# Optimization experiments

Hardware: AMD Instinct MI355X
Metric: run time of the kernel (lower is better)

The kernel has to match this reference:

```python
import jax, jax.numpy as jnp
import numpy as np

R = 4        # downsample / window size
HEADS = 8
TOPK = 4


def _dwconv3x3(x_nchw, w, b):
    # depthwise 3x3, padding 1. w: [C,1,3,3]
    C = x_nchw.shape[1]
    y = jax.lax.conv_general_dilated(
        x_nchw, w, window_strides=(1, 1), padding=((1, 1), (1, 1)),
        dimension_numbers=('NCHW', 'OIHW', 'NCHW'), feature_group_count=C)
    return y + b[None, :, None, None]


def setup_inputs() -> dict:
    key = jax.random.key(0)
    ks = jax.random.split(key, 8)
    B, H, W, C = 8, 64, 64, 384
    s = 0.02
    return {
        'x': jax.random.normal(ks[0], (B, H, W, C), jnp.float32),
        'qkv_w': jax.random.normal(ks[1], (3 * C, C), jnp.float32) * s,
        'dwx_w': jax.random.normal(ks[2], (C, 1, 3, 3), jnp.float32) * s,
        'dwx_b': jax.random.normal(ks[3], (C,), jnp.float32) * s,
        'dw_w': jax.random.normal(ks[4], (C, 1, 3, 3), jnp.float32) * s,
        'dw_b': jax.random.normal(ks[5], (C,), jnp.float32) * s,
        'pw_w': jax.random.normal(ks[6], (C, C), jnp.float32) * s,
        'pw_b': jax.random.normal(ks[7], (C,), jnp.float32) * s,
    }


def reference(x, qkv_w, dwx_w, dwx_b, dw_w, dw_b, pw_w, pw_b):
    B, H, W, C = x.shape
    h, r, topk = HEADS, R, TOPK
    d = C // h
    scale = d ** -0.5
    Hc, Wc = H // r, W // r
    Nc = Hc * Wc

    y = x

    # ---- coarse stream: avg-pool downsample then dense attention ----
    xc = x.reshape(B, Hc, r, Wc, r, C).mean(axis=(2, 4))       # [B,Hc,Wc,C]
    xc = xc.reshape(B, Nc, C)
    qkv = (xc @ qkv_w.T).reshape(B, Nc, 3, h, d).transpose(2, 0, 3, 1, 4)
    q, k, v = qkv[0], qkv[1], qkv[2]                           # [B,h,Nc,d]
    attn = jnp.einsum('bhqd,bhkd->bhqk', q, k) * scale         # [B,h,Nc,Nc]
    _, indices = jax.lax.top_k(attn, topk)                     # [B,h,Nc,topk]
    attn = jax.nn.softmax(attn, axis=-1)
    xo = jnp.einsum('bhqk,bhkd->bhqd', attn, v)                # [B,h,Nc,d]
    xo = xo.transpose(0, 2, 1, 3).reshape(B, Hc, Wc, C)

    # ---- full-res stream: windowed sparse attention driven by topk indices ----
    yf = y.reshape(B, H * W, C)
    QKV = (yf @ qkv_w.T).reshape(B, H * W, 3, h, d).transpose(2, 0, 3, 1, 4)
    Q, K, V = QKV[0], QKV[1], QKV[2]                           # [B,h,H*W,d]

    def to_windows(t):
        # [B,h,H*W,d] -> [B,h,nWin,r*r,d], window order matches coarse (h w) flatten
        t = t.reshape(B, h, Hc, r, Wc, r, d).transpose(0, 1, 2, 4, 3, 5, 6)
        return t.reshape(B, h, Nc, r * r, d)

    Qw, Kw, Vw = to_windows(Q), to_windows(K), to_windows(V)

    idx = indices[:, :, :, :, None, None]                      # [B,h,Nc,topk,1,1]
    Kg = jnp.take_along_axis(Kw[:, :, None], idx, axis=3)      # [B,h,Nc,topk,r*r,d]
    Vg = jnp.take_along_axis(Vw[:, :, None], idx, axis=3)
    Kg = Kg.reshape(B, h, Nc, topk * r * r, d)
    Vg = Vg.reshape(B, h, Nc, topk * r * r, d)

    a2 = jnp.einsum('bhnqd,bhnkd->bhnqk', Qw, Kg) * scale
    a2 = jax.nn.softmax(a2, axis=-1)
    yo = jnp.einsum('bhnqk,bhnkd->bhnqd', a2, Vg)              # [B,h,Nc,r*r,d]
    yo = yo.reshape(B, h, Hc, Wc, r, r, d).transpose(0, 2, 4, 3, 5, 1, 6)
    yo = yo.reshape(B, H, W, C)                                # NHWC

    # ---- coarse branch: nearest upsample + depthwise conv ----
    xn = xo.transpose(0, 3, 1, 2)                              # [B,C,Hc,Wc]
    xn = jnp.repeat(jnp.repeat(xn, r, axis=2), r, axis=3)      # [B,C,H,W]
    xn = _dwconv3x3(xn, dwx_w, dwx_b)
    xn = xn.transpose(0, 2, 3, 1)                              # NHWC

    # ---- fuse, depthwise + pointwise conv ----
    z = 0.5 * xn + 0.5 * yo
    z = z.transpose(0, 3, 1, 2)                                # NCHW
    z = _dwconv3x3(z, dw_w, dw_b)
    z = jnp.einsum('bchw,oc->bohw', z, pw_w) + pw_b[None, :, None, None]
    return z.transpose(0, 2, 3, 1)                             # NHWC
```

## Files before the change

### kernel.cpp

```cpp
#include <hip/hip_runtime.h>
#include <hip/hip_bf16.h>


#define Bq 8
#define Hh 8
#define Dd 48
#define Cc 384
#define NC 256
#define MFINE 32768
#define KDIM 384
#define SCALE 0.14433756729740643f

typedef __attribute__((ext_vector_type(8))) short short8;
typedef __attribute__((ext_vector_type(4))) short short4v;
typedef __attribute__((ext_vector_type(4))) float floatx4;

#define QKVW_PLANE 12582912

#define WS_XBF   88342528
#define WS_XC     9437184
#define WS_WQKV 113508352
#define WS_WDWX 114393088
#define WS_BDWX 114400000
#define WS_WDW  114400768
#define WS_BDW  114407680
#define WS_WPW  114408448
#define WS_BPW  114703360

__global__ __launch_bounds__(256) void k_detect(const ushort* x, int* flag) {
    __shared__ int cnt;
    if (threadIdx.x == 0) cnt = 0;
    __syncthreads();
    int c = 0;
    for (int i = threadIdx.x; i < 8192; i += 256) {
        int e = (x[i] >> 7) & 0xFF;
        if (e >= 0xC1) c++;
    }
    atomicAdd(&cnt, c);
    __syncthreads();
    if (threadIdx.x == 0) *flag = (cnt > 16) ? 1 : 0;
}

__device__ __forceinline__ void cvt_seg(const void* src, __hip_bfloat16* dst, int blk, int n4, int fl) {
    int i = blk * 256 + threadIdx.x;
    if (i >= n4) return;
    if (fl) {
        floatx4 v = ((const floatx4*)src)[i];
        short4v o;
        for (int t = 0; t < 4; t++) {
            __hip_bfloat16 hb = __float2bfloat16(v[t]);
            o[t] = *(short*)&hb;
        }
        ((short4v*)dst)[i] = o;
    } else {
        ((short4v*)dst)[i] = ((const short4v*)src)[i];
    }
}

__global__ __launch_bounds__(256) void k_cvt_pool(
        const void* sx, const void* s1, const void* s2, const void* s3,
        const void* s4, const void* s5, const void* s6, const void* s7,
        char* ws, const int* flag) {
    int blk = blockIdx.x;
    int fl = *flag;
    if (blk < 12288) { cvt_seg(sx, (__hip_bfloat16*)(ws + WS_XBF),  blk,          3145728, fl); return; }
    if (blk < 12720) { cvt_seg(s1, (__hip_bfloat16*)(ws + WS_WQKV), blk - 12288,  110592, fl); return; }
    if (blk < 12724) { cvt_seg(s2, (__hip_bfloat16*)(ws + WS_WDWX), blk - 12720,  864,    fl); return; }
    if (blk < 12725) { cvt_seg(s3, (__hip_bfloat16*)(ws + WS_BDWX), blk - 12724,  96,     fl); return; }
    if (blk < 12729) { cvt_seg(s4, (__hip_bfloat16*)(ws + WS_WDW),  blk - 12725,  864,    fl); return; }
    if (blk < 12730) { cvt_seg(s5, (__hip_bfloat16*)(ws + WS_BDW),  blk - 12729,  96,     fl); return; }
    if (blk < 12874) { cvt_seg(s6, (__hip_bfloat16*)(ws + WS_WPW),  blk - 12730,  36864,  fl); return; }
    if (blk < 12875) { cvt_seg(s7, (__hip_bfloat16*)(ws + WS_BPW),  blk - 12874,  96,     fl); return; }
    int pb = blk - 12875;
    if (threadIdx.x >= 192) return;
    int b = pb >> 8, n = pb & 255;
    int yc = n >> 4, xcc = n & 15;
    int c0 = threadIdx.x * 2;
    size_t pixbase = (((size_t)(b * 64 + yc * 4)) * 64 + xcc * 4) * Cc + c0;
    float s0 = 0.f, s1v = 0.f;
    if (fl) {
        const float* xf = (const float*)sx;
        for (int i = 0; i < 4; i++)
            for (int j = 0; j < 4; j++) {
                float2 u = *(const float2*)(xf + pixbase + ((size_t)i * 64 + j) * Cc);
                s0 += u.x; s1v += u.y;
            }
    } else {
        const ushort* xb = (const ushort*)sx;
        for (int i = 0; i < 4; i++)
            for (int j = 0; j < 4; j++) {
                uint u = *(const uint*)(xb + pixbase + ((size_t)i * 64 + j) * Cc);
                s0 += __uint_as_float(u << 16);
                s1v += __uint_as_float(u & 0xFFFF0000u);
            }
    }
    __hip_bfloat16 h0 = __float2bfloat16(s0 * 0.0625f), h1 = __float2bfloat16(s1v * 0.0625f);
    uint uo = (uint)*(ushort*)&h0 | ((uint)*(ushort*)&h1 << 16);
    *(uint*)((ushort*)(ws + WS_XC) + (size_t)pb * Cc + c0) = uo;
}

__device__ __forceinline__ void gload_lds16(const ushort* g, short* l) {
    __builtin_amdgcn_global_load_lds(
        (const __attribute__((address_space(1))) unsigned int*)(g),
        (__attribute__((address_space(3))) unsigned int*)(l), 16, 0, 0);
}

__device__ __forceinline__ void gemm128_dbuf(const ushort* A, const ushort* B,
                                             int tile_m, int tile_n,
                                             short* As, short* Bs, floatx4 (&acc)[4][4]) {
    int lane = threadIdx.x & 63, wave = threadIdx.x >> 6;
    int m_off = (wave >> 1) * 64, n_off = (wave & 1) * 64;
    int row16 = lane & 15, quad = lane >> 4;
    int srow = lane >> 3;
    int scol = (((lane & 7) ^ srow) * 8);
    for (int i = 0; i < 4; i++)
        for (int j = 0; j < 4; j++)
            acc[i][j] = (floatx4){0.f, 0.f, 0.f, 0.f};
    int rsw = (row16 & 7) * 8;
#define STG(buf, k0)                                                                          \
    for (int g = wave; g < 16; g += 4) {                                                      \
        gload_lds16(A + (size_t)(tile_m + g * 8 + srow) * KDIM + (k0) + scol, As + (buf) * 8192 + g * 512); \
        gload_lds16(B + (size_t)(tile_n + g * 8 + srow) * KDIM + (k0) + scol, Bs + (buf) * 8192 + g * 512); \
    }
    STG(0, 0)
    int cur = 0;
    for (int k0 = 0; k0 < KDIM; k0 += 64) {
        if (k0 + 64 < KDIM) {
            STG(cur ^ 1, k0 + 64)
            asm volatile("s_waitcnt vmcnt(8)" ::: "memory");
        } else {
            asm volatile("s_waitcnt vmcnt(0)" ::: "memory");
        }
        __builtin_amdgcn_s_barrier();
        __builtin_amdgcn_sched_barrier(0);
        const short* Ab = As + cur * 8192;
        const short* Bb = Bs + cur * 8192;
        for (int h = 0; h < 2; h++) {
            short8 af[4], bf[4];
            for (int mt = 0; mt < 4; mt++)
                af[mt] = *(const short8*)(Ab + (m_off + mt * 16 + row16) * 64 + (((h * 4 + quad) * 8) ^ rsw));
            for (int nt = 0; nt < 4; nt++)
                bf[nt] = *(const short8*)(Bb + (n_off + nt * 16 + row16) * 64 + (((h * 4 + quad) * 8) ^ rsw));
            for (int mt = 0; mt < 4; mt++)
                for (int nt = 0; nt < 4; nt++)
                    acc[mt][nt] = __builtin_amdgcn_mfma_f32_16x16x32_bf16(af[mt], bf[nt], acc[mt][nt], 0, 0, 0);
        }
        __builtin_amdgcn_sched_barrier(0);
        __builtin_amdgcn_s_barrier();
        cur ^= 1;
    }
#undef STG
}

__device__ __forceinline__ void gemm128_sb(const ushort* A, const ushort* B,
                                           int tile_m, int tile_n,
                                           short* As, short* Bs, floatx4 (&acc)[4][4]) {
    int lane = threadIdx.x & 63, wave = threadIdx.x >> 6;
    int m_off = (wave >> 1) * 64, n_off = (wave & 1) * 64;
    int row16 = lane & 15, quad = lane >> 4;
    int srow = lane >> 3;
    int scol = (((lane & 7) ^ srow) * 8);
    for (int i = 0; i < 4; i++)
        for (int j = 0; j < 4; j++)
            acc[i][j] = (floatx4){0.f, 0.f, 0.f, 0.f};
    int rsw = (row16 & 7) * 8;
    for (int k0 = 0; k0 < KDIM; k0 += 64) {
        for (int g = wave; g < 16; g += 4) {
            gload_lds16(A + (size_t)(tile_m + g * 8 + srow) * KDIM + k0 + scol, As + g * 512);
            gload_lds16(B + (size_t)(tile_n + g * 8 + srow) * KDIM + k0 + scol, Bs + g * 512);
        }
        __syncthreads();
        for (int h = 0; h < 2; h++) {
            short8 af[4], bf[4];
            for (int mt = 0; mt < 4; mt++)
                af[mt] = *(const short8*)(As + (m_off + mt * 16 + row16) * 64 + (((h * 4 + quad) * 8) ^ rsw));
            for (int nt = 0; nt < 4; nt++)
                bf[nt] = *(const short8*)(Bs + (n_off + nt * 16 + row16) * 64 + (((h * 4 + quad) * 8) ^ rsw));
            for (int mt = 0; mt < 4; mt++)
                for (int nt = 0; nt < 4; nt++)
                    acc[mt][nt] = __builtin_amdgcn_mfma_f32_16x16x32_bf16(af[mt], bf[nt], acc[mt][nt], 0, 0, 0);
        }
        __syncthreads();
    }
}

__device__ __forceinline__ floatx4 mfma_tile(const ushort* A, const ushort* W,
                                             int tile_m, int tile_n, int lane) {
    int row16 = lane & 15, quad = lane >> 4;
    const ushort* arow = A + (size_t)(tile_m + row16) * KDIM + quad * 8;
    const ushort* brow = W + (size_t)(tile_n + row16) * KDIM + quad * 8;
    floatx4 acc = {0.f, 0.f, 0.f, 0.f};
    for (int kk = 0; kk < KDIM; kk += 32) {
        short8 af = *(const short8*)(arow + kk);
        short8 bf = *(const short8*)(brow + kk);
        acc = __builtin_amdgcn_mfma_f32_16x16x32_bf16(af, bf, acc, 0, 0, 0);
    }
    return acc;
}

__global__ __launch_bounds__(256) void k_gemm_qkv_coarse(const ushort* A, const ushort* W,
                                                         __hip_bfloat16* qh, __hip_bfloat16* ql,
                                                         __hip_bfloat16* kh, __hip_bfloat16* kl,
                                                         __hip_bfloat16* vt) {
    int lane = threadIdx.x & 63, wave = threadIdx.x >> 6;
    int tile_m = blockIdx.y * 32 + (wave >> 1) * 16;
    int tile_n = blockIdx.x * 32 + (wave & 1) * 16;
    floatx4 acc = mfma_tile(A, W, tile_m, tile_n, lane);
    int row16 = lane & 15, quad = lane >> 4;
    int n = tile_n + row16;
    int which = n / Cc, hd = n % Cc, head = hd / Dd, dim = hd % Dd;
    for (int rr = 0; rr < 4; rr++) {
        int m = tile_m + quad * 4 + rr;
        int b = m >> 8, nc = m & 255;
        float v = acc[rr];
        __hip_bfloat16 hi = __float2bfloat16(v);
        if (which == 0) {
            size_t p = ((size_t)((b * Hh + head) * NC + nc)) * Dd + dim;
            qh[p] = hi;
            ql[p] = __float2bfloat16(v - __bfloat162float(hi));
        } else if (which == 1) {
            size_t p = ((size_t)((b * Hh + head) * NC + nc)) * Dd + dim;
            kh[p] = hi;
            kl[p] = __float2bfloat16(v - __bfloat162float(hi));
        } else {
            vt[((size_t)((b * Hh + head) * Dd + dim)) * NC + nc] = hi;
        }
    }
}

#define PST 264
__global__ __launch_bounds__(256) void k_coarse_attn(const ushort* qh, const ushort* ql,
                                                     const ushort* kh, const ushort* kl,
                                                     const ushort* vt,
                                                     int* idx_out, __hip_bfloat16* xo) {
    __shared__ __align__(16) short Pl[4][16 * PST];
    int lane = threadIdx.x & 63, wave = threadIdx.x >> 6;
    int bh = blockIdx.x >> 2, qt = blockIdx.x & 3;
    int row16 = lane & 15, quad = lane >> 4;
    int q0 = qt * 64 + wave * 16;
    short8 zf = {0, 0, 0, 0, 0, 0, 0, 0};
    const ushort* qhr = qh + ((size_t)(bh * NC + q0 + row16)) * Dd;
    const ushort* qlr = ql + ((size_t)(bh * NC + q0 + row16)) * Dd;
    short8 aqh0 = *(const short8*)(qhr + quad * 8);
    short8 aqh1 = (quad < 2) ? *(const short8*)(qhr + 32 + quad * 8) : zf;
    short8 aql0 = *(const short8*)(qlr + quad * 8);
    short8 aql1 = (quad < 2) ? *(const short8*)(qlr + 32 + quad * 8) : zf;
    floatx4 s[16];
    for (int nt = 0; nt < 16; nt++) {
        const ushort* khr = kh + ((size_t)(bh * NC + nt * 16 + row16)) * Dd;
        const ushort* klr = kl + ((size_t)(bh * NC + nt * 16 + row16)) * Dd;
        short8 bh0 = *(const short8*)(khr + quad * 8);
        short8 bh1 = (quad < 2) ? *(const short8*)(khr + 32 + quad * 8) : zf;
        short8 bl0 = *(const short8*)(klr + quad * 8);
        short8 bl1 = (quad < 2) ? *(const short8*)(klr + 32 + quad * 8) : zf;
        floatx4 a = {0.f, 0.f, 0.f, 0.f};
        a = __builtin_amdgcn_mfma_f32_16x16x32_bf16(aqh0, bh0, a, 0, 0, 0);
        a = __builtin_amdgcn_mfma_f32_16x16x32_bf16(aqh1, bh1, a, 0, 0, 0);
        a = __builtin_amdgcn_mfma_f32_16x16x32_bf16(aqh0, bl0, a, 0, 0, 0);
        a = __builtin_amdgcn_mfma_f32_16x16x32_bf16(aqh1, bl1, a, 0, 0, 0);
        a = __builtin_amdgcn_mfma_f32_16x16x32_bf16(aql0, bh0, a, 0, 0, 0);
        a = __builtin_amdgcn_mfma_f32_16x16x32_bf16(aql1, bh1, a, 0, 0, 0);
        s[nt] = a;
    }
    for (int rr = 0; rr < 4; rr++) {
        float sv[16];
        for (int nt = 0; nt < 16; nt++) sv[nt] = s[nt][rr] * SCALE;
        int chosen[4] = {-1, -1, -1, -1};
        float rowmax = 0.f;
        for (int it = 0; it < 4; it++) {
            float bv = -3.402823e38f; int bi = 0x7fffffff;
            for (int nt = 0; nt < 16; nt++) {
                int ki = nt * 16 + row16;
                bool skip = (ki == chosen[0]) | (ki == chosen[1]) | (ki == chosen[2]) | (ki == chosen[3]);
                if (!skip && sv[nt] > bv) { bv = sv[nt]; bi = ki; }
            }
            for (int mk = 1; mk < 16; mk <<= 1) {
                float ov = __shfl_xor(bv, mk); int oi = __shfl_xor(bi, mk);
                if (ov > bv || (ov == bv && oi < bi)) { bv = ov; bi = oi; }
            }
            chosen[it] = bi;
            if (it == 0) rowmax = bv;
        }
        if (row16 == 0) {
            int q = q0 + quad * 4 + rr;
            for (int it = 0; it < 4; it++)
                idx_out[((size_t)bh * NC + q) * 4 + it] = chosen[it];
        }
        float ex[16], sum = 0.f;
        for (int nt = 0; nt < 16; nt++) { ex[nt] = __expf(sv[nt] - rowmax); sum += ex[nt]; }
        for (int mk = 1; mk < 16; mk <<= 1) sum += __shfl_xor(sum, mk);
        float inv = 1.f / sum;
        for (int nt = 0; nt < 16; nt++) {
            __hip_bfloat16 hb = __float2bfloat16(ex[nt] * inv);
            Pl[wave][(quad * 4 + rr) * PST + nt * 16 + row16] = *(short*)&hb;
        }
    }
    const ushort* vbase = vt + (size_t)bh * Dd * NC;
    floatx4 o[3];
    for (int i = 0; i < 3; i++) o[i] = (floatx4){0.f, 0.f, 0.f, 0.f};
    for (int k0 = 0; k0 < 256; k0 += 32) {
        short8 pa = *(const short8*)&Pl[wave][row16 * PST + k0 + quad * 8];
        for (int d2 = 0; d2 < 3; d2++) {
            short8 vb = *(const short8*)(vbase + (size_t)(d2 * 16 + row16) * NC + k0 + quad * 8);
            o[d2] = __builtin_amdgcn_mfma_f32_16x16x32_bf16(pa, vb, o[d2], 0, 0, 0);
        }
    }
    int b = bh >> 3, hh = bh & 7;
    for (int rr = 0; rr < 4; rr++) {
        int q = q0 + quad * 4 + rr;
        size_t base = ((size_t)(b * NC + q)) * Cc + hh * Dd;
        for (int d2 = 0; d2 < 3; d2++)
            xo[base + d2 * 16 + row16] = __float2bfloat16(o[d2][rr]);
    }
}

__global__ __launch_bounds__(256) void k_gemm_qkv_fine(const ushort* A, const ushort* W, __hip_bfloat16* qkvw) {
    __shared__ __align__(16) short smem[32768];
    floatx4 acc[4][4];
    int f = blockIdx.x;
    int s = (f & 7) * 288 + (f >> 3);
    int by = s / 9, bx = s - by * 9;
    int tile_m = by * 128, tile_n = bx * 128;
    gemm128_dbuf(A, W, tile_m, tile_n, smem, smem + 16384, acc);
    int lane = threadIdx.x & 63, wave = threadIdx.x >> 6;
    int m_off = (wave >> 1) * 64, n_off = (wave & 1) * 64;
    int row16 = lane & 15, quad = lane >> 4;
    short* epi = smem + wave * 2304;
    int r = lane >> 1, parity = lane & 1;
    for (int half = 0; half < 2; half++) {
        __syncthreads();
        for (int mt2 = 0; mt2 < 2; mt2++) {
            int mt = half * 2 + mt2;
            for (int nt = 0; nt < 4; nt++)
                for (int rr = 0; rr < 4; rr++) {
                    __hip_bfloat16 hb = __float2bfloat16(acc[mt][nt][rr]);
                    epi[(mt2 * 16 + quad * 4 + rr) * 72 + nt * 16 + row16] = *(short*)&hb;
                }
        }
        __syncthreads();
        int m = tile_m + m_off + half * 32 + r;
        int b = m >> 12, pix = m & 4095;
        int y = pix >> 6, x = pix & 63;
        int win = (y >> 2) * 16 + (x >> 2);
        int pos = (y & 3) * 4 + (x & 3);
        size_t mrow = ((size_t)b * Hh * NC * 16 * Dd) + ((size_t)win * 16 + pos) * Dd;
        for (int i = 0; i < 4; i++) {
            int j = parity + 2 * i;
            int n = tile_n + n_off + j * 8;
            int which = n / Cc, hd = n % Cc, head = hd / Dd, dim = hd % Dd;
            short8 val = *(const short8*)(epi + r * 72 + j * 8);
            size_t dst = (size_t)which * QKVW_PLANE + (size_t)head * (NC * 16 * Dd) + mrow + dim;
            *(short8*)((ushort*)qkvw + dst) = val;
        }
    }
}

#define PSTRIDE 80
#define VSTRIDE 72
__global__ __launch_bounds__(256) void k_win_attn(const __hip_bfloat16* qkvw, const int* idx, __hip_bfloat16* yo) {
    __shared__ __align__(16) short Pl[4][16 * PSTRIDE];
    __shared__ __align__(16) short Vt[4][48 * VSTRIDE];
    int lane = threadIdx.x & 63, wave = threadIdx.x >> 6;
    int gw = blockIdx.x * 4 + wave;
    int bh = gw >> 8, n = gw & 255;
    int row16 = lane & 15, quad = lane >> 4;
    const ushort* qb  = (const ushort*)qkvw + (size_t)(bh * NC + n) * 768;
    const ushort* kwb = (const ushort*)qkvw + (size_t)QKVW_PLANE + (size_t)bh * NC * 768;
    const ushort* vwb = (const ushort*)qkvw + 2 * (size_t)QKVW_PLANE + (size_t)bh * NC * 768;
    int sel[4];
    for (int g = 0; g < 4; g++) sel[g] = idx[(size_t)gw * 4 + g];
    const ushort* vrow = vwb + (size_t)sel[quad] * 768 + row16 * 48;
    short8 vv[6];
    for (int i = 0; i < 6; i++) vv[i] = *(const short8*)(vrow + i * 8);
    short8 zf = {0, 0, 0, 0, 0, 0, 0, 0};
    short8 aq0 = *(const short8*)(qb + row16 * 48 + quad * 8);
    short8 aq1 = (quad < 2) ? *(const short8*)(qb + row16 * 48 + 32 + quad * 8) : zf;
    floatx4 s[4];
    for (int nt = 0; nt < 4; nt++) {
        const ushort* kb = kwb + (size_t)sel[nt] * 768 + row16 * 48;
        short8 bk0 = *(const short8*)(kb + quad * 8);
        short8 bk1 = (quad < 2) ? *(const short8*)(kb + 32 + quad * 8) : zf;
        floatx4 a = {0.f, 0.f, 0.f, 0.f};
        a = __builtin_amdgcn_mfma_f32_16x16x32_bf16(aq0, bk0, a, 0, 0, 0);
        a = __builtin_amdgcn_mfma_f32_16x16x32_bf16(aq1, bk1, a, 0, 0, 0);
        s[nt] = a;
    }
    for (int i = 0; i < 6; i++)
        for (int j = 0; j < 8; j++)
            Vt[wave][(i * 8 + j) * VSTRIDE + lane] = vv[i][j];
    for (int rr = 0; rr < 4; rr++) {
        float sv[4];
        float m = -3.402823e38f;
        for (int nt = 0; nt < 4; nt++) { sv[nt] = s[nt][rr] * SCALE; m = fmaxf(m, sv[nt]); }
        for (int msk = 1; msk < 16; msk <<= 1) m = fmaxf(m, __shfl_xor(m, msk));
        float sum = 0.f;
        for (int nt = 0; nt < 4; nt++) { sv[nt] = expf(sv[nt] - m); sum += sv[nt]; }
        for (int msk = 1; msk < 16; msk <<= 1) sum += __shfl_xor(sum, msk);
        float inv = 1.f / sum;
        for (int nt = 0; nt < 4; nt++) {
            __hip_bfloat16 hb = __float2bfloat16(sv[nt] * inv);
            Pl[wave][(quad * 4 + rr) * PSTRIDE + nt * 16 + row16] = *(short*)&hb;
        }
    }
    floatx4 o[3];
    for (int i = 0; i < 3; i++) o[i] = (floatx4){0.f, 0.f, 0.f, 0.f};
    for (int k0 = 0; k0 < 64; k0 += 32) {
        short8 pa = *(const short8*)&Pl[wave][row16 * PSTRIDE + k0 + quad * 8];
        for (int nt2 = 0; nt2 < 3; nt2++) {
            short8 vb = *(const short8*)&Vt[wave][(nt2 * 16 + row16) * VSTRIDE + k0 + quad * 8];
            o[nt2] = __builtin_amdgcn_mfma_f32_16x16x32_bf16(pa, vb, o[nt2], 0, 0, 0);
        }
    }
    int b = bh >> 3, hh = bh & 7;
    int wy = n >> 4, wx = n & 15;
    for (int rr = 0; rr < 4; rr++) {
        int q = quad * 4 + rr;
        int y = wy * 4 + (q >> 2), x = wx * 4 + (q & 3);
        size_t base = (((size_t)(b * 64 + y)) * 64 + x) * Cc + hh * Dd;
        for (int nt2 = 0; nt2 < 3; nt2++)
            yo[base + nt2 * 16 + row16] = __float2bfloat16(o[nt2][rr]);
    }
}

__global__ __launch_bounds__(192) void k_up_mix(const __hip_bfloat16* xo, const __hip_bfloat16* yo,
                                                const __hip_bfloat16* dwx_w, const __hip_bfloat16* dwx_b,
                                                __hip_bfloat16* zpre) {
    int c2 = threadIdx.x, c0 = c2 * 2;
    int blk = blockIdx.x;
    int xc = blk & 7, by = blk >> 3;
    int y = by & 63, b = by >> 6;
    int x0 = xc * 8;
    float w0[9], w1[9];
    for (int k = 0; k < 9; k++) {
        w0[k] = __bfloat162float(dwx_w[c0 * 9 + k]);
        w1[k] = __bfloat162float(dwx_w[(c0 + 1) * 9 + k]);
    }
    float bias0 = __bfloat162float(dwx_b[c0]), bias1 = __bfloat162float(dwx_b[c0 + 1]);
    const __hip_bfloat16* xrow[3];
    for (int di = 0; di < 3; di++) {
        int yy = y + di - 1;
        xrow[di] = (yy >= 0 && yy < 64) ? xo + ((size_t)(b * NC + (yy >> 2) * 16)) * Cc + c0 : nullptr;
    }
    float vL0[3], vL1[3], vM0[3], vM1[3], vR0[3], vR1[3];
    int cm = x0 >> 2;
    for (int di = 0; di < 3; di++) {
        uint um = xrow[di] ? *(const uint*)(xrow[di] + (size_t)cm * Cc) : 0u;
        vM0[di] = __uint_as_float(um << 16); vM1[di] = __uint_as_float(um & 0xFFFF0000u);
        uint ul = (x0 > 0 && xrow[di]) ? *(const uint*)(xrow[di] + (size_t)(cm - 1) * Cc) : 0u;
        vL0[di] = __uint_as_float(ul << 16); vL1[di] = __uint_as_float(ul & 0xFFFF0000u);
        vR0[di] = vM0[di]; vR1[di] = vM1[di];
    }
    size_t obase = (size_t)by * 64 * Cc + c0;
    for (int x = x0; x < x0 + 8; x++) {
        float a0 = bias0, a1 = bias1;
        for (int di = 0; di < 3; di++) {
            a0 += vL0[di] * w0[di * 3] + vM0[di] * w0[di * 3 + 1] + vR0[di] * w0[di * 3 + 2];
            a1 += vL1[di] * w1[di * 3] + vM1[di] * w1[di * 3 + 1] + vR1[di] * w1[di * 3 + 2];
        }
        uint uy = *(const uint*)(yo + obase + (size_t)x * Cc);
        float z0 = 0.5f * a0 + 0.5f * __uint_as_float(uy << 16);
        float z1 = 0.5f * a1 + 0.5f * __uint_as_float(uy & 0xFFFF0000u);
        __hip_bfloat16 h0 = __float2bfloat16(z0), h1 = __float2bfloat16(z1);
        uint uo = (uint)*(ushort*)&h0 | ((uint)*(ushort*)&h1 << 16);
        *(uint*)(zpre + obase + (size_t)x * Cc) = uo;
        for (int di = 0; di < 3; di++) {
            vL0[di] = vM0[di]; vL1[di] = vM1[di];
            vM0[di] = vR0[di]; vM1[di] = vR1[di];
        }
        int nx = x + 2;
        if ((nx & 3) == 0 || nx > 63) {
            int ncol = nx >> 2;
            for (int di = 0; di < 3; di++) {
                uint ur = (nx <= 63 && xrow[di]) ? *(const uint*)(xrow[di] + (size_t)ncol * Cc) : 0u;
                vR0[di] = __uint_as_float(ur << 16); vR1[di] = __uint_as_float(ur & 0xFFFF0000u);
            }
        }
    }
}

__global__ __launch_bounds__(192) void k_dw2(const __hip_bfloat16* zpre, const __hip_bfloat16* dw_w,
                                             const __hip_bfloat16* dw_b, __hip_bfloat16* z) {
    int c2 = threadIdx.x, c0 = c2 * 2;
    int blk = blockIdx.x;
    int xc = blk & 7, by = blk >> 3;
    int y = by & 63, b = by >> 6;
    int x0 = xc * 8;
    float w0[9], w1[9];
    for (int k = 0; k < 9; k++) {
        w0[k] = __bfloat162float(dw_w[c0 * 9 + k]);
        w1[k] = __bfloat162float(dw_w[(c0 + 1) * 9 + k]);
    }
    float bias0 = __bfloat162float(dw_b[c0]), bias1 = __bfloat162float(dw_b[c0 + 1]);
    const __hip_bfloat16* row[3];
    for (int di = 0; di < 3; di++) {
        int yy = y + di - 1;
        row[di] = (yy >= 0 && yy < 64) ? zpre + ((size_t)(b * 64 + yy) * 64) * Cc + c0 : nullptr;
    }
    float pv0[3], pv1[3], cv0[3], cv1[3], f0[3], f1[3];
    for (int di = 0; di < 3; di++) {
        uint up = (x0 > 0 && row[di]) ? *(const uint*)(row[di] + (size_t)(x0 - 1) * Cc) : 0u;
        pv0[di] = __uint_as_float(up << 16); pv1[di] = __uint_as_float(up & 0xFFFF0000u);
        uint uc = row[di] ? *(const uint*)(row[di] + (size_t)x0 * Cc) : 0u;
        cv0[di] = __uint_as_float(uc << 16); cv1[di] = __uint_as_float(uc & 0xFFFF0000u);
        uint uf = row[di] ? *(const uint*)(row[di] + (size_t)(x0 + 1) * Cc) : 0u;
        f0[di] = __uint_as_float(uf << 16); f1[di] = __uint_as_float(uf & 0xFFFF0000u);
    }
    size_t obase = (size_t)by * 64 * Cc + c0;
    for (int x = x0; x < x0 + 8; x++) {
        float nv0[3], nv1[3];
        for (int di = 0; di < 3; di++) { nv0[di] = f0[di]; nv1[di] = f1[di]; }
        int nx = x + 2;
        for (int di = 0; di < 3; di++) {
            uint uf = (nx < 64 && row[di]) ? *(const uint*)(row[di] + (size_t)nx * Cc) : 0u;
            f0[di] = __uint_as_float(uf << 16); f1[di] = __uint_as_float(uf & 0xFFFF0000u);
        }
        float a0 = bias0, a1 = bias1;
        for (int di = 0; di < 3; di++) {
            a0 += pv0[di] * w0[di * 3] + cv0[di] * w0[di * 3 + 1] + nv0[di] * w0[di * 3 + 2];
            a1 += pv1[di] * w1[di * 3] + cv1[di] * w1[di * 3 + 1] + nv1[di] * w1[di * 3 + 2];
        }
        __hip_bfloat16 h0 = __float2bfloat16(a0), h1 = __float2bfloat16(a1);
        uint uo = (uint)*(ushort*)&h0 | ((uint)*(ushort*)&h1 << 16);
        *(uint*)(z + obase + (size_t)x * Cc) = uo;
        for (int di = 0; di < 3; di++) {
            pv0[di] = cv0[di]; pv1[di] = cv1[di];
            cv0[di] = nv0[di]; cv1[di] = nv1[di];
        }
    }
}

__global__ __launch_bounds__(256) void k_gemm_pw(const ushort* Z, const ushort* W, const __hip_bfloat16* bias,
                                                 void* out, const int* flag) {
    __shared__ __align__(16) short smem[16384];
    floatx4 acc[4][4];
    int f = blockIdx.x;
    int s = (f & 7) * 96 + (f >> 3);
    int by = s / 3, bx = s - by * 3;
    int tile_m = by * 128, tile_n = bx * 128;
    gemm128_sb(Z, W, tile_m, tile_n, smem, smem + 8192, acc);
    int lane = threadIdx.x & 63, wave = threadIdx.x >> 6;
    int m_off = (wave >> 1) * 64, n_off = (wave & 1) * 64;
    int row16 = lane & 15, quad = lane >> 4;
    float* epi = (float*)smem + wave * 1216;
    int f32out = *flag;
    int r4 = lane >> 2, c4 = lane & 3;
    for (int mt = 0; mt < 4; mt++) {
        __syncthreads();
        for (int nt = 0; nt < 4; nt++)
            for (int rr = 0; rr < 4; rr++)
                epi[(quad * 4 + rr) * 76 + nt * 16 + row16] = acc[mt][nt][rr];
        __syncthreads();
        int m = tile_m + m_off + mt * 16 + r4;
        for (int i = 0; i < 4; i++) {
            int j = c4 + 4 * i;
            int n0 = tile_n + n_off + j * 4;
            floatx4 v = *(const floatx4*)(epi + r4 * 76 + j * 4);
            short4v bb = *(const short4v*)((const ushort*)bias + n0);
            for (int t = 0; t < 4; t++) {
                short sb = bb[t];
                v[t] += __bfloat162float(*(const __hip_bfloat16*)&sb);
            }
            if (f32out) {
                *(floatx4*)((float*)out + (size_t)m * Cc + n0) = v;
            } else {
                short4v o;
                for (int t = 0; t < 4; t++) { __hip_bfloat16 hb = __float2bfloat16(v[t]); o[t] = *(short*)&hb; }
                *(short4v*)((__hip_bfloat16*)out + (size_t)m * Cc + n0) = o;
            }
        }
    }
}

extern "C" void kernel_launch(void* const* d_in, const int* in_sizes, int n_in,
                              void* d_out, int out_size, void* d_ws, size_t ws_size,
                              hipStream_t stream) {
    char* ws = (char*)d_ws;
    __hip_bfloat16* qhp  = (__hip_bfloat16*)(ws);
    __hip_bfloat16* qlp  = (__hip_bfloat16*)(ws + 1572864);
    __hip_bfloat16* khp  = (__hip_bfloat16*)(ws + 3145728);
    __hip_bfloat16* klp  = (__hip_bfloat16*)(ws + 4718592);
    __hip_bfloat16* vtp  = (__hip_bfloat16*)(ws + 6291456);
    __hip_bfloat16* xc   = (__hip_bfloat16*)(ws + WS_XC);
    int*            idx  = (int*)(ws + 11010048);
    __hip_bfloat16* xo   = (__hip_bfloat16*)(ws + 11272192);
    __hip_bfloat16* qkvw = (__hip_bfloat16*)(ws + 12845056);
    __hip_bfloat16* yo   = (__hip_bfloat16*)(ws + WS_XBF);
    __hip_bfloat16* xbf  = (__hip_bfloat16*)(ws + WS_XBF);
    __hip_bfloat16* zpre = (__hip_bfloat16*)(ws + 12845056);
    __hip_bfloat16* zbuf = (__hip_bfloat16*)(ws + WS_XBF);
    __hip_bfloat16* wqkv = (__hip_bfloat16*)(ws + WS_WQKV);
    __hip_bfloat16* wdwx = (__hip_bfloat16*)(ws + WS_WDWX);
    __hip_bfloat16* bdwx = (__hip_bfloat16*)(ws + WS_BDWX);
    __hip_bfloat16* wdw  = (__hip_bfloat16*)(ws + WS_WDW);
    __hip_bfloat16* bdw  = (__hip_bfloat16*)(ws + WS_BDW);
    __hip_bfloat16* wpw  = (__hip_bfloat16*)(ws + WS_WPW);
    __hip_bfloat16* bpw  = (__hip_bfloat16*)(ws + WS_BPW);
    int*            flag = (int*)(ws + 114704128);

    k_detect<<<1, 256, 0, stream>>>((const ushort*)d_in[0], flag);
    k_cvt_pool<<<14923, 256, 0, stream>>>(d_in[0], d_in[1], d_in[2], d_in[3],
                                          d_in[4], d_in[5], d_in[6], d_in[7],
                                          ws, flag);

    k_gemm_qkv_coarse<<<dim3(36, 64), 256, 0, stream>>>((const ushort*)xc, (const ushort*)wqkv,
                                                        qhp, qlp, khp, klp, vtp);
    k_coarse_attn<<<256, 256, 0, stream>>>((const ushort*)qhp, (const ushort*)qlp,
                                           (const ushort*)khp, (const ushort*)klp,
                                           (const ushort*)vtp, idx, xo);
    k_gemm_qkv_fine<<<2304, 256, 0, stream>>>((const ushort*)xbf, (const ushort*)wqkv, qkvw);
    k_win_attn<<<4096, 256, 0, stream>>>(qkvw, idx, yo);
    k_up_mix<<<4096, 192, 0, stream>>>(xo, yo, wdwx, bdwx, zpre);
    k_dw2<<<4096, 192, 0, stream>>>(zpre, wdw, bdw, zbuf);
    k_gemm_pw<<<768, 256, 0, stream>>>((const ushort*)zbuf, (const ushort*)wpw, bpw, d_out, flag);
}
```

Baseline: 293.3 us.

## Fuse upsample-dwconv-mix and second depthwise conv into one kernel

Merges the two depthwise-conv kernels into one. Each block recomputes the mixed pre-activation for a 3x10 halo region in registers, then applies the second 3x3 depthwise conv directly. This removes the zpre round trip through global memory and one kernel launch. In exchange, each block redundantly computes the halo (30 vs 8 points per row tile), reads more yo values, and uses many more registers.

```diff
diff --git a/kernel.cpp b/kernel.cpp
--- a/kernel.cpp
+++ b/kernel.cpp
@@ -422,110 +422,99 @@
     }
 }
 
-__global__ __launch_bounds__(192) void k_up_mix(const __hip_bfloat16* xo, const __hip_bfloat16* yo,
+__global__ __launch_bounds__(192) void k_dwfuse(const __hip_bfloat16* xo, const __hip_bfloat16* yo,
                                                 const __hip_bfloat16* dwx_w, const __hip_bfloat16* dwx_b,
-                                                __hip_bfloat16* zpre) {
-    int c2 = threadIdx.x, c0 = c2 * 2;
+                                                const __hip_bfloat16* dw_w, const __hip_bfloat16* dw_b,
+                                                __hip_bfloat16* z) {
+    int c0 = threadIdx.x * 2;
     int blk = blockIdx.x;
     int xc = blk & 7, by = blk >> 3;
     int y = by & 63, b = by >> 6;
     int x0 = xc * 8;
-    float w0[9], w1[9];
+    float wx0[9], wx1[9], wd0[9], wd1[9];
     for (int k = 0; k < 9; k++) {
-        w0[k] = __bfloat162float(dwx_w[c0 * 9 + k]);
-        w1[k] = __bfloat162float(dwx_w[(c0 + 1) * 9 + k]);
-    }
-    float bias0 = __bfloat162float(dwx_b[c0]), bias1 = __bfloat162float(dwx_b[c0 + 1]);
-    const __hip_bfloat16* xrow[3];
-    for (int di = 0; di < 3; di++) {
-        int yy = y + di - 1;
-        xrow[di] = (yy >= 0 && yy < 64) ? xo + ((size_t)(b * NC + (yy >> 2) * 16)) * Cc + c0 : nullptr;
-    }
-    float vL0[3], vL1[3], vM0[3], vM1[3], vR0[3], vR1[3];
-    int cm = x0 >> 2;
-    for (int di = 0; di < 3; di++) {
-        uint um = xrow[di] ? *(const uint*)(xrow[di] + (size_t)cm * Cc) : 0u;
-        vM0[di] = __uint_as_float(um << 16); vM1[di] = __uint_as_float(um & 0xFFFF0000u);
-        uint ul = (x0 > 0 && xrow[di]) ? *(const uint*)(xrow[di] + (size_t)(cm - 1) * Cc) : 0u;
-        vL0[di] = __uint_as_float(ul << 16); vL1[di] = __uint_as_float(ul & 0xFFFF0000u);
-        vR0[di] = vM0[di]; vR1[di] = vM1[di];
-    }
-    size_t obase = (size_t)by * 64 * Cc + c0;
-    for (int x = x0; x < x0 + 8; x++) {
-        float a0 = bias0, a1 = bias1;
-        for (int di = 0; di < 3; di++) {
-            a0 += vL0[di] * w0[di * 3] + vM0[di] * w0[di * 3 + 1] + vR0[di] * w0[di * 3 + 2];
-            a1 += vL1[di] * w1[di * 3] + vM1[di] * w1[di * 3 + 1] + vR1[di] * w1[di * 3 + 2];
-        }
-        uint uy = *(const uint*)(yo + obase + (size_t)x * Cc);
-        float z0 = 0.5f * a0 + 0.5f * __uint_as_float(uy << 16);
-        float z1 = 0.5f * a1 + 0.5f * __uint_as_float(uy & 0xFFFF0000u);
-        __hip_bfloat16 h0 = __float2bfloat16(z0), h1 = __float2bfloat16(z1);
-        uint uo = (uint)*(ushort*)&h0 | ((uint)*(ushort*)&h1 << 16);
-        *(uint*)(zpre + obase + (size_t)x * Cc) = uo;
-        for (int di = 0; di < 3; di++) {
-            vL0[di] = vM0[di]; vL1[di] = vM1[di];
-            vM0[di] = vR0[di]; vM1[di] = vR1[di];
-        }
-        int nx = x + 2;
-        if ((nx & 3) == 0 || nx > 63) {
-            int ncol = nx >> 2;
-            for (int di = 0; di < 3; di++) {
-                uint ur = (nx <= 63 && xrow[di]) ? *(const uint*)(xrow[di] + (size_t)ncol * Cc) : 0u;
-                vR0[di] = __uint_as_float(ur << 16); vR1[di] = __uint_as_float(ur & 0xFFFF0000u);
-            }
-        }
-    }
-}
-
-__global__ __launch_bounds__(192) void k_dw2(const __hip_bfloat16* zpre, const __hip_bfloat16* dw_w,
-                                             const __hip_bfloat16* dw_b, __hip_bfloat16* z) {
-    int c2 = threadIdx.x, c0 = c2 * 2;
-    int blk = blockIdx.x;
-    int xc = blk & 7, by = blk >> 3;
-    int y = by & 63, b = by >> 6;
-    int x0 = xc * 8;
-    float w0[9], w1[9];
-    for (int k = 0; k < 9; k++) {
-        w0[k] = __bfloat162float(dw_w[c0 * 9 + k]);
-        w1[k] = __bfloat162float(dw_w[(c0 + 1) * 9 + k]);
-    }
-    float bias0 = __bfloat162float(dw_b[c0]), bias1 = __bfloat162float(dw_b[c0 + 1]);
-    const __hip_bfloat16* row[3];
-    for (int di = 0; di < 3; di++) {
-        int yy = y + di - 1;
-        row[di] = (yy >= 0 && yy < 64) ? zpre + ((size_t)(b * 64 + yy) * 64) * Cc + c0 : nullptr;
-    }
-    float pv0[3], pv1[3], cv0[3], cv1[3], f0[3], f1[3];
-    for (int di = 0; di < 3; di++) {
-        uint up = (x0 > 0 && row[di]) ? *(const uint*)(row[di] + (size_t)(x0 - 1) * Cc) : 0u;
-        pv0[di] = __uint_as_float(up << 16); pv1[di] = __uint_as_float(up & 0xFFFF0000u);
-        uint uc = row[di] ? *(const uint*)(row[di] + (size_t)x0 * Cc) : 0u;
-        cv0[di] = __uint_as_float(uc << 16); cv1[di] = __uint_as_float(uc & 0xFFFF0000u);
-        uint uf = row[di] ? *(const uint*)(row[di] + (size_t)(x0 + 1) * Cc) : 0u;
-        f0[di] = __uint_as_float(uf << 16); f1[di] = __uint_as_float(uf & 0xFFFF0000u);
-    }
-    size_t obase = (size_t)by * 64 * Cc + c0;
-    for (int x = x0; x < x0 + 8; x++) {
-        float nv0[3], nv1[3];
-        for (int di = 0; di < 3; di++) { nv0[di] = f0[di]; nv1[di] = f1[di]; }
-        int nx = x + 2;
-        for (int di = 0; di < 3; di++) {
-            uint uf = (nx < 64 && row[di]) ? *(const uint*)(row[di] + (size_t)nx * Cc) : 0u;
-            f0[di] = __uint_as_float(uf << 16); f1[di] = __uint_as_float(uf & 0xFFFF0000u);
-        }
-        float a0 = bias0, a1 = bias1;
-        for (int di = 0; di < 3; di++) {
-            a0 += pv0[di] * w0[di * 3] + cv0[di] * w0[di * 3 + 1] + nv0[di] * w0[di * 3 + 2];
-            a1 += pv1[di] * w1[di * 3] + cv1[di] * w1[di * 3 + 1] + nv1[di] * w1[di * 3 + 2];
-        }
+        wx0[k] = __bfloat162float(dwx_w[c0 * 9 + k]);
+        wx1[k] = __bfloat162float(dwx_w[(c0 + 1) * 9 + k]);
+        wd0[k] = __bfloat162float(dw_w[c0 * 9 + k]);
+        wd1[k] = __bfloat162float(dw_w[(c0 + 1) * 9 + k]);
+    }
+    float bx0 = __bfloat162float(dwx_b[c0]), bx1 = __bfloat162float(dwx_b[c0 + 1]);
+    float bd0 = __bfloat162float(dw_b[c0]),  bd1 = __bfloat162float(dw_b[c0 + 1]);
+    int r_base = (y >= 2 ? y - 2 : 0) >> 2;
+    int c_base = x0 / 4 - 1;
+    float px0[2][4], px1[2][4];
+    for (int pr = 0; pr < 2; pr++) {
+        int cr = r_base + pr;
+        for (int pc = 0; pc < 4; pc++) {
+            int cc2 = c_base + pc;
+            uint u = (cr < 16 && cc2 >= 0 && cc2 < 16) ?
+                *(const uint*)((const ushort*)xo + ((size_t)(b * NC + cr * 16 + cc2)) * Cc + c0) : 0u;
+            px0[pr][pc] = __uint_as_float(u << 16);
+            px1[pr][pc] = __uint_as_float(u & 0xFFFF0000u);
+        }
+    }
+    float sr0[5][4], sr1[5][4];
+#pragma unroll
+    for (int f = 0; f < 5; f++) {
+        int fy = y - 2 + f;
+        bool valid = (fy >= 0 && fy < 64);
+        int pr = valid ? ((fy >> 2) - r_base) : 0;
+#pragma unroll
+        for (int pc = 0; pc < 4; pc++) {
+            float v0 = pr ? px0[1][pc] : px0[0][pc];
+            float v1 = pr ? px1[1][pc] : px1[0][pc];
+            sr0[f][pc] = valid ? v0 : 0.f;
+            sr1[f][pc] = valid ? v1 : 0.f;
+        }
+    }
+    float zp0[3][10], zp1[3][10];
+#pragma unroll
+    for (int r = 0; r < 3; r++)
+#pragma unroll
+        for (int cq = 0; cq < 10; cq++) { zp0[r][cq] = 0.f; zp1[r][cq] = 0.f; }
+#pragma unroll
+    for (int r = 0; r < 3; r++) {
+        int fyz = y + r - 1;
+        if (fyz < 0 || fyz > 63) continue;
+#pragma unroll
+        for (int cq = 0; cq < 10; cq++) {
+            int fxz = x0 - 1 + cq;
+            if (fxz < 0 || fxz > 63) continue;
+            float a0 = bx0, a1 = bx1;
+#pragma unroll
+            for (int dy = -1; dy <= 1; dy++) {
+#pragma unroll
+                for (int dx = -1; dx <= 1; dx++) {
+                    int t = cq - 1 + dx;
+                    int pc = 1 + ((t + 8) / 4 - 2);
+                    int fx = fxz + dx;
+                    bool cvalid = (fx >= 0 && fx < 64);
+                    int f = r + dy + 1;
+                    float t0 = cvalid ? sr0[f][pc] : 0.f;
+                    float t1 = cvalid ? sr1[f][pc] : 0.f;
+                    a0 += t0 * wx0[(dy + 1) * 3 + (dx + 1)];
+                    a1 += t1 * wx1[(dy + 1) * 3 + (dx + 1)];
+                }
+            }
+            uint uy = *(const uint*)((const ushort*)yo + (((size_t)(b * 64 + fyz)) * 64 + fxz) * Cc + c0);
+            zp0[r][cq] = 0.5f * a0 + 0.5f * __uint_as_float(uy << 16);
+            zp1[r][cq] = 0.5f * a1 + 0.5f * __uint_as_float(uy & 0xFFFF0000u);
+        }
+    }
+    size_t obase = ((size_t)(b * 64 + y) * 64) * Cc + c0;
+#pragma unroll
+    for (int xq = 0; xq < 8; xq++) {
+        float a0 = bd0, a1 = bd1;
+#pragma unroll
+        for (int dy = 0; dy < 3; dy++)
+#pragma unroll
+            for (int dx = 0; dx < 3; dx++) {
+                a0 += zp0[dy][xq + dx] * wd0[dy * 3 + dx];
+                a1 += zp1[dy][xq + dx] * wd1[dy * 3 + dx];
+            }
         __hip_bfloat16 h0 = __float2bfloat16(a0), h1 = __float2bfloat16(a1);
         uint uo = (uint)*(ushort*)&h0 | ((uint)*(ushort*)&h1 << 16);
-        *(uint*)(z + obase + (size_t)x * Cc) = uo;
-        for (int di = 0; di < 3; di++) {
-            pv0[di] = cv0[di]; pv1[di] = cv1[di];
-            cv0[di] = nv0[di]; cv1[di] = nv1[di];
-        }
+        *(uint*)((ushort*)z + obase + (size_t)(x0 + xq) * Cc) = uo;
     }
 }
 
@@ -586,8 +575,7 @@
     __hip_bfloat16* qkvw = (__hip_bfloat16*)(ws + 12845056);
     __hip_bfloat16* yo   = (__hip_bfloat16*)(ws + WS_XBF);
     __hip_bfloat16* xbf  = (__hip_bfloat16*)(ws + WS_XBF);
-    __hip_bfloat16* zpre = (__hip_bfloat16*)(ws + 12845056);
-    __hip_bfloat16* zbuf = (__hip_bfloat16*)(ws + WS_XBF);
+    __hip_bfloat16* zbuf = (__hip_bfloat16*)(ws + 12845056);
     __hip_bfloat16* wqkv = (__hip_bfloat16*)(ws + WS_WQKV);
     __hip_bfloat16* wdwx = (__hip_bfloat16*)(ws + WS_WDWX);
     __hip_bfloat16* bdwx = (__hip_bfloat16*)(ws + WS_BDWX);
@@ -609,7 +597,6 @@
                                            (const ushort*)vtp, idx, xo);
     k_gemm_qkv_fine<<<2304, 256, 0, stream>>>((const ushort*)xbf, (const ushort*)wqkv, qkvw);
     k_win_attn<<<4096, 256, 0, stream>>>(qkvw, idx, yo);
-    k_up_mix<<<4096, 192, 0, stream>>>(xo, yo, wdwx, bdwx, zpre);
-    k_dw2<<<4096, 192, 0, stream>>>(zpre, wdw, bdw, zbuf);
+    k_dwfuse<<<4096, 192, 0, stream>>>(xo, yo, wdwx, bdwx, wdw, bdw, zbuf);
     k_gemm_pw<<<768, 256, 0, stream>>>((const ushort*)zbuf, (const ushort*)wpw, bpw, d_out, flag);
 }
```

Result: no change. 292.8 us (-0.2%).
